# Optimization experiments

Measured on AMD Instinct MI355X. Metric: run time of the kernel, lower is better.

The kernel has to match this reference:

```python
import jax, jax.numpy as jnp
import numpy as np

B, T, D = 32, 200, 256
H, DH = 4, 32
INNER = H * DH  # 128
L, FF, NI = 8, 1024, 100000
NB = 64  # gap/recency buckets


def _ln(x, g, b, eps=1e-5):
    m = x.mean(-1, keepdims=True)
    v = jnp.mean((x - m) ** 2, -1, keepdims=True)
    return (x - m) / jnp.sqrt(v + eps) * g + b


def _gelu(x):
    return jax.nn.gelu(x, approximate=False)


def _dwconv_causal(x, w, b):
    # x: [B,T,C], w: [C,k] depthwise kernel, causal left-pad (k-1)
    k = w.shape[1]
    xp = jnp.pad(x, ((0, 0), (k - 1, 0), (0, 0))).transpose(0, 2, 1)  # [B,C,T+k-1]
    out = jax.lax.conv_general_dilated(
        xp, w[:, None, :], (1,), 'VALID',
        dimension_numbers=('NCH', 'OIH', 'NCH'), feature_group_count=w.shape[0])
    return out.transpose(0, 2, 1) + b


def _causal_linear_attention(q, k, v, m4):
    q = (jax.nn.elu(q) + 1.0) * m4
    k = (jax.nn.elu(k) + 1.0) * m4
    v = v * m4
    kv = jnp.einsum('bthd,bthe->bthde', k, v)          # [B,T,H,DH,DH]
    kv_prefix = jnp.cumsum(kv, axis=1)
    k_prefix = jnp.cumsum(k, axis=1)
    num = jnp.einsum('bthd,bthde->bthe', q, kv_prefix)
    den = jnp.sum(q * k_prefix, -1, keepdims=True)
    return num / (den + 1e-6) * m4


def _forward(item_emb, pos_emb, gap_emb, rec_emb, tf_w1, tf_b1, tf_w2, tf_b2,
             in_g, in_b, l_ln1g, l_ln1b, l_win, l_bin, l_wc, l_bc, l_tw, l_tb,
             l_pw, l_pb, l_wmix, l_bmix, l_ln2g, l_ln2b, l_wf1, l_bf1, l_wf2, l_bf2,
             fn_g, fn_b, pg_w, pg_b, uh_w1, uh_b1, uh_lng, uh_lnb, uh_w2, uh_b2,
             item_bias, ids, ts, lens):
    Bb, Tt = ids.shape
    pos = jnp.arange(Tt)
    mask = pos[None, :] >= (Tt - lens)[:, None]  # right-aligned valid mask [B,T]
    prev_ts = jnp.roll(ts, 1, axis=1)
    prev_mask = jnp.roll(mask, 1, axis=1).at[:, 0].set(False)
    zero = jnp.zeros_like(ts)
    gap_vals = jnp.where(mask & prev_mask, jnp.maximum(ts - prev_ts, 0), zero)
    latest = ts[:, -1:]
    rec_vals = jnp.where(mask, jnp.maximum(latest - ts, 0), zero)

    def buck(v, n):
        vf = jnp.maximum(v.astype(jnp.float32), 0.0)
        return jnp.clip(jnp.floor(jnp.log2(vf + 1.0)), 0, n - 1).astype(jnp.int32)

    gb = buck(gap_vals, NB)
    rb = buck(rec_vals, NB)
    rec_raw = jnp.maximum(latest - ts, 0).astype(jnp.float32)
    tf = jnp.stack([jnp.log1p(gb.astype(jnp.float32)), jnp.log1p(rec_raw)], -1)  # [B,T,2]
    dense_time = _gelu(tf @ tf_w1 + tf_b1) @ tf_w2 + tf_b2

    x = item_emb[ids] + pos_emb[None] + gap_emb[gb] + rec_emb[rb] + dense_time
    mf = mask[..., None].astype(x.dtype)
    m4 = mask[..., None, None].astype(x.dtype)
    x = _ln(x, in_g, in_b) * mf

    for i in range(L):
        res = x
        nrm = _ln(x, l_ln1g[i], l_ln1b[i])
        proj = nrm @ l_win[i] + l_bin[i]  # [B,T,D+3*INNER]
        gate = proj[..., :D]
        q = proj[..., D:D + INNER].reshape(Bb, Tt, H, DH)
        k = proj[..., D + INNER:D + 2 * INNER].reshape(Bb, Tt, H, DH)
        v = proj[..., D + 2 * INNER:].reshape(Bb, Tt, H, DH)
        content = _causal_linear_attention(q, k, v, m4).reshape(Bb, Tt, INNER) @ l_wc[i] + l_bc[i]
        temporal = _dwconv_causal(nrm, l_tw[i], l_tb[i])
        positional = _dwconv_causal(nrm, l_pw[i], l_pb[i])
        mixed = jnp.concatenate([content, temporal, positional], -1) @ l_wmix[i] + l_bmix[i]
        x = (res + jax.nn.sigmoid(gate) * mixed) * mf
        h = _ln(x, l_ln2g[i], l_ln2b[i])
        ffn = _gelu(h @ l_wf1[i] + l_bf1[i]) @ l_wf2[i] + l_bf2[i]
        x = (x + ffn) * mf

    x = _ln(x, fn_g, fn_b) * mf
    denom = jnp.maximum(lens, 1)[:, None].astype(x.dtype)
    mean_pooled = (x * mf).sum(1) / denom
    ps = (x @ pg_w + pg_b)[..., 0]
    ps = jnp.where(mask, ps, -1e9)
    pw = jax.nn.softmax(ps, axis=1)[..., None]
    attn_pooled = (pw * x).sum(1)
    last = x[:, -1, :]
    u = jnp.concatenate([last, mean_pooled, attn_pooled], -1)
    u = _gelu(u @ uh_w1 + uh_b1)
    u = _ln(u, uh_lng, uh_lnb)
    u = u @ uh_w2 + uh_b2
    u = u / jnp.maximum(jnp.linalg.norm(u, axis=-1, keepdims=True), 1e-12)
    ie = item_emb[1:]
    ie = ie / jnp.maximum(jnp.linalg.norm(ie, axis=-1, keepdims=True), 1e-12)
    return u @ ie.T + item_bias[1:]


def setup_inputs() -> dict:
    key = jax.random.key(0)
    it = iter(jax.random.split(key, 64))
    def nk():
        return next(it)
    def w(*s):
        return jax.random.normal(nk(), s, jnp.float32) * 0.02
    inp = dict(
        history_ids=jax.random.randint(nk(), (B, T), 0, NI),
        history_timestamps=jnp.sort(jax.random.randint(nk(), (B, T), 0, 1000000), axis=1),
        history_lengths=jax.random.randint(nk(), (B,), 1, T + 1),
        item_emb=w(NI + 1, D).at[0].set(0.0),
        pos_emb=w(T, D), gap_emb=w(NB, D), rec_emb=w(NB, D),
        tf_w1=w(2, D), tf_b1=jnp.zeros((D,)), tf_w2=w(D, D), tf_b2=jnp.zeros((D,)),
        in_g=jnp.ones((D,)), in_b=jnp.zeros((D,)),
        l_ln1g=jnp.ones((L, D)), l_ln1b=jnp.zeros((L, D)),
        l_win=w(L, D, D + 3 * INNER), l_bin=jnp.zeros((L, D + 3 * INNER)),
        l_wc=w(L, INNER, D), l_bc=jnp.zeros((L, D)),
        l_tw=w(L, D, 3), l_tb=jnp.zeros((L, D)),
        l_pw=w(L, D, 5), l_pb=jnp.zeros((L, D)),
        l_wmix=w(L, 3 * D, D), l_bmix=jnp.zeros((L, D)),
        l_ln2g=jnp.ones((L, D)), l_ln2b=jnp.zeros((L, D)),
        l_wf1=w(L, D, FF), l_bf1=jnp.zeros((L, FF)),
        l_wf2=w(L, FF, D), l_bf2=jnp.zeros((L, D)),
        fn_g=jnp.ones((D,)), fn_b=jnp.zeros((D,)),
        pg_w=w(D, 1), pg_b=jnp.zeros((1,)),
        uh_w1=w(3 * D, 1024), uh_b1=jnp.zeros((1024,)),
        uh_lng=jnp.ones((1024,)), uh_lnb=jnp.zeros((1024,)),
        uh_w2=w(1024, D), uh_b2=jnp.zeros((D,)),
        item_bias=jnp.zeros((NI + 1,)),
    )
    return inp


def reference(history_ids, history_timestamps, history_lengths, item_emb, pos_emb,
              gap_emb, rec_emb, tf_w1, tf_b1, tf_w2, tf_b2, in_g, in_b, l_ln1g,
              l_ln1b, l_win, l_bin, l_wc, l_bc, l_tw, l_tb, l_pw, l_pb, l_wmix,
              l_bmix, l_ln2g, l_ln2b, l_wf1, l_bf1, l_wf2, l_bf2, fn_g, fn_b,
              pg_w, pg_b, uh_w1, uh_b1, uh_lng, uh_lnb, uh_w2, uh_b2, item_bias):
    return _forward(item_emb, pos_emb, gap_emb, rec_emb, tf_w1, tf_b1, tf_w2, tf_b2,
                    in_g, in_b, l_ln1g, l_ln1b, l_win, l_bin, l_wc, l_bc, l_tw, l_tb,
                    l_pw, l_pb, l_wmix, l_bmix, l_ln2g, l_ln2b, l_wf1, l_bf1, l_wf2,
                    l_bf2, fn_g, fn_b, pg_w, pg_b, uh_w1, uh_b1, uh_lng, uh_lnb,
                    uh_w2, uh_b2, item_bias, history_ids, history_timestamps,
                    history_lengths)
```

## Files before the change

kernel.cpp:

```cpp
#include <hip/hip_runtime.h>
#include <math.h>

#define B_ 32
#define T_ 200
#define D_ 256
#define H_ 4
#define DH_ 32
#define INNER_ 128
#define L_ 8
#define FF_ 1024
#define NI_ 100000
#define NB_ 64
#define CH_ 25

typedef __attribute__((ext_vector_type(8))) short short8;
typedef __attribute__((ext_vector_type(8))) unsigned short ushort8;
typedef __attribute__((ext_vector_type(4))) unsigned short ushort4v;
typedef __attribute__((ext_vector_type(4))) float floatx4;

__device__ __forceinline__ float gelu_f(float x){
  return 0.5f*x*(1.0f+erff(x*0.70710678118654752f));
}
__device__ __forceinline__ float wsum(float v){
  #pragma unroll
  for (int o=32;o>0;o>>=1) v += __shfl_xor(v,o,64);
  return v;
}
__device__ __forceinline__ unsigned short f2bf(float x){
  unsigned int u = __float_as_uint(x);
  unsigned int r = (u + 0x7fffu + ((u>>16)&1u)) >> 16;
  return (unsigned short)r;
}
__device__ __forceinline__ float bf2f(unsigned short u){
  return __uint_as_float(((unsigned int)u)<<16);
}

__device__ __forceinline__ void cvt_tile(const float* __restrict__ src, unsigned short* __restrict__ dst,
                                         int K, int N, int tk, int tn, int tid, float (*s)[33])
{
  int tx = tid & 31, ty0 = tid >> 5;
  #pragma unroll
  for (int it=0; it<4; ++it){
    int ty = ty0 + it*8;
    s[ty][tx] = src[(size_t)(tk*32+ty)*N + tn*32+tx];
  }
  __syncthreads();
  #pragma unroll
  for (int it=0; it<4; ++it){
    int ty = ty0 + it*8;
    dst[(size_t)(tn*32+ty)*K + tk*32 + tx] = f2bf(s[tx][ty]);
  }
}

__global__ __launch_bounds__(256) void k_cvtAll(
  const float* __restrict__ win, const float* __restrict__ wmix,
  const float* __restrict__ wf1, const float* __restrict__ wf2,
  const float* __restrict__ tfw2, const float* __restrict__ uhw1, const float* __restrict__ uhw2,
  unsigned short* __restrict__ WtPerm, unsigned short* __restrict__ WtMixT,
  unsigned short* __restrict__ WtH)
{
  __shared__ float s[32][33];
  int b = blockIdx.x, tid = threadIdx.x;
  if (b < 6912){
    int l = b / 864, r = b % 864;
    if (r < 160)      cvt_tile(win + (size_t)l*163840, WtPerm + (size_t)l*688128,          256, 640,  r/20,      r%20,      tid, s);
    else if (r < 352){int t=r-160; cvt_tile(wmix + (size_t)l*196608, WtMixT + (size_t)l*196608, 768, 256, t/8, t%8, tid, s);}
    else if (r < 608){int t=r-352; cvt_tile(wf1 + (size_t)l*262144, WtPerm + (size_t)l*688128 + 163840, 256, 1024, t/32, t%32, tid, s);}
    else             {int t=r-608; cvt_tile(wf2 + (size_t)l*262144, WtPerm + (size_t)l*688128 + 425984, 1024, 256, t/8, t%8, tid, s);}
  } else {
    int r = b - 6912;
    if (r < 64)       cvt_tile(tfw2, WtH,        256, 256,  r/8,  r%8,  tid, s);
    else if (r < 832){int t=r-64;  cvt_tile(uhw1, WtH+65536,  768, 1024, t/32, t%32, tid, s);}
    else             {int t=r-832; cvt_tile(uhw2, WtH+851968, 1024, 256, t/8,  t%8,  tid, s);}
  }
}

__global__ __launch_bounds__(256) void k_asm(
  const float* __restrict__ WcombF, const unsigned short* __restrict__ WtMixT,
  unsigned short* __restrict__ WtBig)
{
  int l = blockIdx.x >> 3, g = blockIdx.x & 7;
  int tid = threadIdx.x;
  int n = g*32 + (tid >> 3);
  int k0 = (tid & 7) * 80;
  const float* wc = WcombF + (size_t)l*32768;
  const unsigned short* wm = WtMixT + (size_t)l*196608 + (size_t)n*768;
  unsigned short* dst = WtBig + (size_t)l*163840 + (size_t)n*640;
  for (int kk=0; kk<80; kk++){
    int k = k0 + kk;
    dst[k] = (k < 128) ? f2bf(wc[(size_t)k*256 + n]) : wm[k+128];
  }
}

__global__ __launch_bounds__(256) void k_bfold(
  const float* __restrict__ bc, const float* __restrict__ bmix,
  const float* __restrict__ wmix, float* __restrict__ bmixP)
{
  int l = blockIdx.x; int n = threadIdx.x;
  const float* w = wmix + (size_t)l*196608;
  const float* c = bc + l*256;
  float s = bmix[l*256 + n];
  for (int d=0; d<256; d++) s += c[d]*w[(size_t)d*256 + n];
  bmixP[l*256+n] = s;
}

template<int TN>
__global__ __launch_bounds__(256) void k_gemm_bf(
    const float* __restrict__ A, const unsigned short* __restrict__ Wt,
    const float* __restrict__ bias, float* __restrict__ C,
    int M, int N, int K, int ldA, int ldW, int ldC, int mode,
    size_t sA, size_t sW, size_t sC, size_t sB)
{
  constexpr int NJ = TN/32;
  __shared__ unsigned short Als[128][40];
  __shared__ unsigned short Bls[TN][40];
  int z = blockIdx.z;
  A += (size_t)z*sA; Wt += (size_t)z*sW; C += (size_t)z*sC;
  const float* bz = bias ? bias + (size_t)z*sB : nullptr;
  int tid = threadIdx.x;
  int wave = tid >> 6, lane = tid & 63;
  int wm = (wave >> 1) * 64, wn = (wave & 1) * (TN/2);
  int frow = lane & 15, kg = lane >> 4;
  int bm = blockIdx.y * 128, bn = blockIdx.x * TN;
  int sm = tid >> 1, skh = (tid & 1) * 16;

  floatx4 acc[4][NJ];
  #pragma unroll
  for (int i=0;i<4;i++)
    #pragma unroll
    for (int j=0;j<NJ;j++) acc[i][j] = (floatx4){0.f,0.f,0.f,0.f};

  for (int k0=0; k0<K; k0+=32){
    {
      int gm = bm + sm;
      float f[16];
      if (gm < M){
        const float4* ap = (const float4*)(A + (size_t)gm*ldA + k0 + skh);
        #pragma unroll
        for (int c=0;c<4;c++){ float4 v = ap[c]; f[c*4]=v.x; f[c*4+1]=v.y; f[c*4+2]=v.z; f[c*4+3]=v.w; }
      } else {
        #pragma unroll
        for (int c=0;c<16;c++) f[c]=0.f;
      }
      ushort8 pa, pb;
      #pragma unroll
      for (int c=0;c<8;c++){ pa[c]=f2bf(f[c]); pb[c]=f2bf(f[8+c]); }
      *(ushort8*)&Als[sm][skh]   = pa;
      *(ushort8*)&Als[sm][skh+8] = pb;
    }
    #pragma unroll
    for (int u=0; u<TN/64; u++){
      int li = tid + u*256;
      int row = li >> 2, koff = (li & 3) * 8;
      int gn = bn + row;
      ushort8 wv;
      if (gn < N){
        wv = *(const ushort8*)&Wt[(size_t)gn*ldW + k0 + koff];
      } else {
        for (int c=0;c<8;c++) wv[c]=0;
      }
      *(ushort8*)&Bls[row][koff] = wv;
    }
    __syncthreads();
    short8 af[4], bf[NJ];
    #pragma unroll
    for (int i=0;i<4;i++) af[i] = *(const short8*)&Als[wm + 16*i + frow][kg*8];
    #pragma unroll
    for (int j=0;j<NJ;j++) bf[j] = *(const short8*)&Bls[wn + 16*j + frow][kg*8];
    #pragma unroll
    for (int i=0;i<4;i++)
      #pragma unroll
      for (int j=0;j<NJ;j++)
        acc[i][j] = __builtin_amdgcn_mfma_f32_16x16x32_bf16(af[i], bf[j], acc[i][j], 0, 0, 0);
    __syncthreads();
  }

  #pragma unroll
  for (int j=0;j<NJ;j++){
    int n = bn + wn + 16*j + frow;
    float bv = bz ? bz[n] : 0.f;
    #pragma unroll
    for (int i=0;i<4;i++){
      int m0 = bm + wm + 16*i + kg*4;
      #pragma unroll
      for (int r=0;r<4;r++){
        int m = m0 + r;
        if (m < M){
          float v = acc[i][j][r] + bv;
          if (mode == 1) v = gelu_f(v);
          float* cp = &C[(size_t)m*ldC + n];
          if (mode == 2) v += *cp;
          *cp = v;
        }
      }
    }
  }
}

template<int K>
__global__ __launch_bounds__(256) void k_gemm16(
    const unsigned short* __restrict__ A, const unsigned short* __restrict__ Wt,
    const float* __restrict__ bias, void* __restrict__ Cv,
    int ldA, int ldW, int ldC, int mode)
{
  int tid = threadIdx.x;
  int wave = tid >> 6, lane = tid & 63;
  int frow = lane & 15, kg = lane >> 4;
  int bm = blockIdx.y * 32;
  int bn = blockIdx.x * 128 + wave * 32;

  const unsigned short* a0 = A + (size_t)(bm + frow)*ldA + kg*8;
  const unsigned short* a1 = a0 + (size_t)16*ldA;
  const unsigned short* b0 = Wt + (size_t)(bn + frow)*ldW + kg*8;
  const unsigned short* b1 = b0 + (size_t)16*ldW;

  floatx4 acc[2][2];
  #pragma unroll
  for (int i=0;i<2;i++)
    #pragma unroll
    for (int j=0;j<2;j++) acc[i][j] = (floatx4){0.f,0.f,0.f,0.f};

  #pragma unroll
  for (int k0=0; k0<K; k0+=32){
    short8 af0 = *(const short8*)(a0 + k0);
    short8 af1 = *(const short8*)(a1 + k0);
    short8 bf0 = *(const short8*)(b0 + k0);
    short8 bf1 = *(const short8*)(b1 + k0);
    acc[0][0] = __builtin_amdgcn_mfma_f32_16x16x32_bf16(af0, bf0, acc[0][0], 0, 0, 0);
    acc[0][1] = __builtin_amdgcn_mfma_f32_16x16x32_bf16(af0, bf1, acc[0][1], 0, 0, 0);
    acc[1][0] = __builtin_amdgcn_mfma_f32_16x16x32_bf16(af1, bf0, acc[1][0], 0, 0, 0);
    acc[1][1] = __builtin_amdgcn_mfma_f32_16x16x32_bf16(af1, bf1, acc[1][1], 0, 0, 0);
  }

  float* Cf = (float*)Cv;
  unsigned short* Ch = (unsigned short*)Cv;
  #pragma unroll
  for (int j=0;j<2;j++){
    int n = bn + 16*j + frow;
    float bv = bias[n];
    #pragma unroll
    for (int i=0;i<2;i++){
      int m0 = bm + 16*i + kg*4;
      #pragma unroll
      for (int r=0;r<4;r++){
        float v = acc[i][j][r] + bv;
        size_t off = (size_t)(m0+r)*ldC + n;
        if (mode == 1)      Cf[off] = gelu_f(v);
        else if (mode == 2) Cf[off] += v;
        else if (mode == 4) Ch[off] = f2bf(gelu_f(v));
        else                Cf[off] = v;
      }
    }
  }
}

template<int K, int MODE>
__global__ __launch_bounds__(256) void k_gemmln(
    const unsigned short* __restrict__ A, const unsigned short* __restrict__ Wt,
    const float* __restrict__ bias, float* __restrict__ xbuf,
    const float* __restrict__ gate, const int* __restrict__ lens,
    const float* __restrict__ g, const float* __restrict__ bb,
    unsigned short* __restrict__ nrm, int maskLN)
{
  __shared__ float rs[32][4];
  __shared__ float rq[32][4];
  int tid = threadIdx.x;
  int wave = tid >> 6, lane = tid & 63;
  int frow = lane & 15, kg = lane >> 4;
  int bm = blockIdx.x * 32;
  int wn = wave * 64;

  const unsigned short* a0 = A + (size_t)(bm + frow)*K + kg*8;
  const unsigned short* a1 = a0 + (size_t)16*K;
  const unsigned short* b0 = Wt + (size_t)(wn + frow)*K + kg*8;

  floatx4 acc[2][4];
  #pragma unroll
  for (int i=0;i<2;i++)
    #pragma unroll
    for (int j=0;j<4;j++) acc[i][j] = (floatx4){0.f,0.f,0.f,0.f};

  #pragma unroll
  for (int k0=0; k0<K; k0+=32){
    short8 af0 = *(const short8*)(a0 + k0);
    short8 af1 = *(const short8*)(a1 + k0);
    #pragma unroll
    for (int j=0;j<4;j++){
      short8 bf = *(const short8*)(b0 + (size_t)16*j*K + k0);
      acc[0][j] = __builtin_amdgcn_mfma_f32_16x16x32_bf16(af0, bf, acc[0][j], 0, 0, 0);
      acc[1][j] = __builtin_amdgcn_mfma_f32_16x16x32_bf16(af1, bf, acc[1][j], 0, 0, 0);
    }
  }

  float xn[2][4][4];
  float rowm[2][4];
  #pragma unroll
  for (int i=0;i<2;i++){
    #pragma unroll
    for (int r=0;r<4;r++){
      int row = bm + 16*i + kg*4 + r;
      int t = row % T_, b = row / T_;
      float m = (t >= T_ - lens[b]) ? 1.f : 0.f;
      rowm[i][r] = m;
      #pragma unroll
      for (int j=0;j<4;j++){
        int n = wn + 16*j + frow;
        float v = acc[i][j][r] + bias[n];
        float xv = xbuf[(size_t)row*256 + n];
        float xnv;
        if (MODE == 0){
          float gv = gate[(size_t)row*640 + n];
          xnv = (xv + v/(1.f+__expf(-gv)))*m;
        } else {
          xnv = (xv + v)*m;
        }
        xn[i][j][r] = xnv;
        xbuf[(size_t)row*256 + n] = xnv;
      }
    }
  }
  float mu[2][4];
  #pragma unroll
  for (int i=0;i<2;i++)
    #pragma unroll
    for (int r=0;r<4;r++){
      float s = xn[i][0][r]+xn[i][1][r]+xn[i][2][r]+xn[i][3][r];
      s += __shfl_xor(s,1,64); s += __shfl_xor(s,2,64);
      s += __shfl_xor(s,4,64); s += __shfl_xor(s,8,64);
      if (frow == 0) rs[16*i + kg*4 + r][wave] = s;
    }
  __syncthreads();
  #pragma unroll
  for (int i=0;i<2;i++)
    #pragma unroll
    for (int r=0;r<4;r++){
      int rl = 16*i + kg*4 + r;
      mu[i][r] = (rs[rl][0]+rs[rl][1]+rs[rl][2]+rs[rl][3]) * (1.f/256.f);
    }
  float rstd[2][4];
  #pragma unroll
  for (int i=0;i<2;i++)
    #pragma unroll
    for (int r=0;r<4;r++){
      float m0 = mu[i][r];
      float s = 0.f;
      #pragma unroll
      for (int j=0;j<4;j++){ float d = xn[i][j][r]-m0; s += d*d; }
      s += __shfl_xor(s,1,64); s += __shfl_xor(s,2,64);
      s += __shfl_xor(s,4,64); s += __shfl_xor(s,8,64);
      if (frow == 0) rq[16*i + kg*4 + r][wave] = s;
    }
  __syncthreads();
  #pragma unroll
  for (int i=0;i<2;i++)
    #pragma unroll
    for (int r=0;r<4;r++){
      int rl = 16*i + kg*4 + r;
      float q = rq[rl][0]+rq[rl][1]+rq[rl][2]+rq[rl][3];
      rstd[i][r] = rsqrtf(q*(1.f/256.f) + 1e-5f);
    }
  #pragma unroll
  for (int i=0;i<2;i++)
    #pragma unroll
    for (int r=0;r<4;r++){
      int row = bm + 16*i + kg*4 + r;
      float ml = maskLN ? rowm[i][r] : 1.f;
      #pragma unroll
      for (int j=0;j<4;j++){
        int n = wn + 16*j + frow;
        float h = (xn[i][j][r]-mu[i][r])*rstd[i][r]*g[n] + bb[n];
        nrm[(size_t)row*256 + n] = f2bf(h*ml);
      }
    }
}

__global__ __launch_bounds__(256) void k_embed(
  const int* __restrict__ ids, const int* __restrict__ ts, const int* __restrict__ lens,
  const float* __restrict__ item_emb, const float* __restrict__ pos_emb,
  const float* __restrict__ gap_emb, const float* __restrict__ rec_emb,
  const float* __restrict__ tf_w1, const float* __restrict__ tf_b1,
  float* __restrict__ xbuf, unsigned short* __restrict__ tfh)
{
  int bt = blockIdx.x;
  int b = bt / T_, t = bt % T_;
  int d = threadIdx.x;
  int len = lens[b];
  int tcur = ts[b*T_+t];
  int tlast = ts[b*T_+T_-1];
  bool mask  = t >= T_ - len;
  bool pmask = (t >= 1) && ((t-1) >= T_ - len);
  int gap = 0;
  if (mask && pmask){ int pv = ts[b*T_+t-1]; gap = max(tcur - pv, 0); }
  int rec = mask ? max(tlast - tcur, 0) : 0;
  int gb = min(max((int)floorf(log2f((float)gap + 1.0f)), 0), NB_-1);
  int rb = min(max((int)floorf(log2f((float)rec + 1.0f)), 0), NB_-1);
  float rec_raw = (float)max(tlast - tcur, 0);
  float tf0 = log1pf((float)gb);
  float tf1 = log1pf(rec_raw);
  float hid = gelu_f(tf0*tf_w1[d] + tf1*tf_w1[D_+d] + tf_b1[d]);
  tfh[(size_t)bt*D_ + d] = f2bf(hid);
  int id = ids[b*T_+t];
  xbuf[(size_t)bt*D_ + d] = item_emb[(size_t)id*D_ + d] + pos_emb[t*D_ + d]
                          + gap_emb[gb*D_ + d] + rec_emb[rb*D_ + d];
}

template<int NC>
__global__ __launch_bounds__(256) void k_ln(
  const float* __restrict__ in, void* __restrict__ out,
  const float* __restrict__ g, const float* __restrict__ bb,
  int rows, const int* __restrict__ lens, int applyMask, int outBf)
{
  int wid = threadIdx.x >> 6, lane = threadIdx.x & 63;
  int r = blockIdx.x*4 + wid;
  if (r >= rows) return;
  const int D = NC*256;
  const float4* rp = (const float4*)(in + (size_t)r*D);
  float4 v[NC];
  float s = 0.f;
  #pragma unroll
  for (int c=0;c<NC;c++){ v[c] = rp[c*64 + lane]; s += v[c].x+v[c].y+v[c].z+v[c].w; }
  s = wsum(s);
  float mean = s / (float)D;
  float q = 0.f;
  #pragma unroll
  for (int c=0;c<NC;c++){
    float a=v[c].x-mean, b2=v[c].y-mean, c2=v[c].z-mean, d2=v[c].w-mean;
// ... 11 lines not shown
    o.x = ((v[c].x-mean)*rstd*gg.x + bv.x)*m;
    o.y = ((v[c].y-mean)*rstd*gg.y + bv.y)*m;
    o.z = ((v[c].z-mean)*rstd*gg.z + bv.z)*m;
    o.w = ((v[c].w-mean)*rstd*gg.w + bv.w)*m;
    if (outBf){
      ushort4v ob; ob.x=f2bf(o.x); ob.y=f2bf(o.y); ob.z=f2bf(o.z); ob.w=f2bf(o.w);
      ((ushort4v*)((unsigned short*)out + (size_t)r*D))[c*64+lane] = ob;
    } else {
      ((float4*)((float*)out + (size_t)r*D))[c*64+lane] = o;
    }
  }
}

__global__ __launch_bounds__(256) void k_lnln(
  float* __restrict__ x, const int* __restrict__ lens,
  const float* __restrict__ g1, const float* __restrict__ b1,
  const float* __restrict__ g2, const float* __restrict__ b2,
  unsigned short* __restrict__ nrm)
{
  int wid = threadIdx.x >> 6, lane = threadIdx.x & 63;
  int r = blockIdx.x*4 + wid;
  int t = r % T_, b = r / T_;
  float m = (t >= T_ - lens[b]) ? 1.f : 0.f;
  float4 v = ((const float4*)(x + (size_t)r*256))[lane];
  float s = wsum(v.x+v.y+v.z+v.w);
  float mean = s/256.f;
  float a=v.x-mean, b2v=v.y-mean, c2=v.z-mean, d2=v.w-mean;
  float q = wsum(a*a+b2v*b2v+c2*c2+d2*d2);
  float rstd = rsqrtf(q/256.f + 1e-5f);
  float4 gg = ((const float4*)g1)[lane];
  float4 bv = ((const float4*)b1)[lane];
  float4 xn;
  xn.x = (a*rstd*gg.x + bv.x)*m;
  xn.y = (b2v*rstd*gg.y + bv.y)*m;
  xn.z = (c2*rstd*gg.z + bv.z)*m;
  xn.w = (d2*rstd*gg.w + bv.w)*m;
  ((float4*)(x + (size_t)r*256))[lane] = xn;
  float s2 = wsum(xn.x+xn.y+xn.z+xn.w);
  float mean2 = s2/256.f;
  float a2=xn.x-mean2, b22=xn.y-mean2, c22=xn.z-mean2, d22=xn.w-mean2;
  float q2 = wsum(a2*a2+b22*b22+c22*c22+d22*d22);
  float rstd2 = rsqrtf(q2/256.f + 1e-5f);
  float4 gg2 = ((const float4*)g2)[lane];
  float4 bv2 = ((const float4*)b2)[lane];
  ushort4v o;
  o.x = f2bf(a2*rstd2*gg2.x + bv2.x);
  o.y = f2bf(b22*rstd2*gg2.y + bv2.y);
  o.z = f2bf(c22*rstd2*gg2.z + bv2.z);
  o.w = f2bf(d22*rstd2*gg2.w + bv2.w);
  ((ushort4v*)(nrm + (size_t)r*256))[lane] = o;
}

__global__ __launch_bounds__(128) void k_attn_sums(
  const float* __restrict__ proj, const int* __restrict__ lens, float* __restrict__ Ssum)
{
  int blk = blockIdx.x;
  int bh = blk >> 3, c = blk & 7;
  int b = bh >> 2, h = bh & 3;
  int tid = threadIdx.x; int e = tid & 31, q = tid >> 5;
  int tstart = T_ - lens[b];
  __shared__ float sk[CH_*32], sv[CH_*32];
  int t0 = c*CH_;
  for (int idx = tid; idx < CH_*32; idx += 128){
    int tl = idx >> 5, dd = idx & 31;
    int t = t0 + tl;
    float m = (t >= tstart) ? 1.f : 0.f;
    const float* pr = proj + (size_t)(b*T_+t)*640 + h*32 + dd;
    float kw = pr[384], vv = pr[512];
    sk[idx] = (kw > 0.f ? kw + 1.f : __expf(kw)) * m;
    sv[idx] = vv * m;
  }
  __syncthreads();
  float acc[8];
  #pragma unroll
  for (int j=0;j<8;j++) acc[j]=0.f;
  for (int tl=0; tl<CH_; tl++){
    const float4* k4 = (const float4*)(sk + tl*32 + q*8);
    float vf = sv[tl*32 + e];
    float4 ka = k4[0], kb = k4[1];
    acc[0]+=ka.x*vf; acc[1]+=ka.y*vf; acc[2]+=ka.z*vf; acc[3]+=ka.w*vf;
    acc[4]+=kb.x*vf; acc[5]+=kb.y*vf; acc[6]+=kb.z*vf; acc[7]+=kb.w*vf;
  }
  float* dst = Ssum + ((size_t)bh*8 + c)*1056;
  #pragma unroll
  for (int j=0;j<8;j++) dst[(q*8+j)*32 + e] = acc[j];
  if (q == 0){
    float s = 0.f;
    for (int tl=0; tl<CH_; tl++) s += sk[tl*32 + e];
    dst[1024 + e] = s;
  }
}

__global__ __launch_bounds__(256) void k_dwpfx(
  const unsigned short* __restrict__ nrm, const float* __restrict__ tw, const float* __restrict__ tb,
  const float* __restrict__ pw, const float* __restrict__ pb, unsigned short* __restrict__ cat,
  float* __restrict__ Ssum)
{
  int bid = blockIdx.x;
  if (bid < 6400){
    int idx = bid*256 + threadIdx.x;
    int d = idx & 255; int bt = idx >> 8; int t = bt % T_;
    float xs[5];
    #pragma unroll
    for (int j=0;j<5;j++){
      int tt = t - 4 + j;
      xs[j] = (tt >= 0) ? bf2f(nrm[(size_t)(bt - 4 + j)*D_ + d]) : 0.f;
    }
    float tmp = tw[d*3+0]*xs[2] + tw[d*3+1]*xs[3] + tw[d*3+2]*xs[4] + tb[d];
    float pos = pb[d];
    #pragma unroll
    for (int j=0;j<5;j++) pos += pw[d*5+j]*xs[j];
    cat[(size_t)bt*640 + 128 + d] = f2bf(tmp);
    cat[(size_t)bt*640 + 384 + d] = f2bf(pos);
  } else {
    int idx = (bid - 6400)*256 + threadIdx.x;
    int bh = idx / 1056, r = idx - bh*1056;
    float* p = Ssum + (size_t)bh*8*1056 + r;
    float s = p[0];
    #pragma unroll
    for (int c=1;c<8;c++){ s += p[(size_t)c*1056]; p[(size_t)c*1056] = s; }
  }
}

__global__ __launch_bounds__(256) void k_attn_out(
  const float* __restrict__ proj, const int* __restrict__ lens,
  const float* __restrict__ Ssum, unsigned short* __restrict__ cat)
{
  int blk = blockIdx.x;
  int bh = blk >> 3, c = blk & 7;
  int b = bh >> 2, h = bh & 3;
  int tid = threadIdx.x; int e = tid & 31, qg = tid >> 5;
  int tstart = T_ - lens[b];
  __shared__ float sq[CH_*32], sk[CH_*32], sv[CH_*32];
  __shared__ float P[1056];
  __shared__ float A[CH_][CH_+1];
  __shared__ float sden[CH_];
  int t0 = c*CH_;
  if (c > 0){
    const float* Pp = Ssum + ((size_t)bh*8 + (c-1))*1056;
    for (int idx = tid; idx < 1056; idx += 256) P[idx] = Pp[idx];
  } else {
    for (int idx = tid; idx < 1056; idx += 256) P[idx] = 0.f;
  }
  for (int idx = tid; idx < CH_*32; idx += 256){
    int tl = idx >> 5, dd = idx & 31;
    int t = t0 + tl;
    float m = (t >= tstart) ? 1.f : 0.f;
    const float* pr = proj + (size_t)(b*T_+t)*640 + h*32 + dd;
    float qv = pr[256], kw = pr[384], vv = pr[512];
    sq[idx] = (qv > 0.f ? qv + 1.f : __expf(qv)) * m;
    sk[idx] = (kw > 0.f ? kw + 1.f : __expf(kw)) * m;
    sv[idx] = vv * m;
  }
  __syncthreads();
  for (int idx = tid; idx < CH_*CH_; idx += 256){
    int t = idx / CH_, tp = idx - t*CH_;
    float s = 0.f;
    if (tp <= t){
      const float4* q4 = (const float4*)(sq + t*32);
      const float4* k4 = (const float4*)(sk + tp*32);
      #pragma unroll
      for (int jj=0;jj<8;jj++){
        float4 qq = q4[jj], kk = k4[jj];
        s += qq.x*kk.x + qq.y*kk.y + qq.z*kk.z + qq.w*kk.w;
      }
    }
    A[t][tp] = s;
  }
  __syncthreads();
  if (tid < CH_){
    int t = tid;
    float s = 0.f;
    for (int tp=0; tp<=t; tp++) s += A[t][tp];
    const float* qf = sq + t*32;
    #pragma unroll
    for (int d=0; d<32; d++) s += qf[d]*P[1024+d];
    sden[t] = s;
  }
  __syncthreads();
  int tlo = (qg*CH_) >> 3, thi = ((qg+1)*CH_) >> 3;
  for (int t = tlo; t < thi; t++){
    float num = 0.f;
    for (int tp=0; tp<=t; tp++) num += A[t][tp]*sv[tp*32+e];
    const float* qf = sq + t*32;
    #pragma unroll
    for (int d=0; d<32; d++) num += qf[d]*P[d*32+e];
    int tg = t0 + t;
    float m = (tg >= tstart) ? 1.f : 0.f;
    cat[(size_t)(b*T_+tg)*640 + h*32 + e] = f2bf(num/(sden[t]+1e-6f)*m);
  }
}

__global__ __launch_bounds__(256) void k_pool(
  const unsigned short* __restrict__ x, const int* __restrict__ lens,
  const float* __restrict__ pg_w, const float* __restrict__ pg_b,
  float* __restrict__ u0)
{
  int b = blockIdx.x;
  int tid = threadIdx.x, wid = tid>>6, lane = tid&63;
  __shared__ float sps[T_];
  __shared__ float spw[T_];
  int len = lens[b]; int tstart = T_ - len;
  const float4* pw4 = (const float4*)pg_w;
  float4 wv = pw4[lane];
  for (int t = wid; t < T_; t += 4){
// ... 133 lines not shown
  const float* l_ln1g = (const float*)d_in[13];
  const float* l_ln1b = (const float*)d_in[14];
  const float* l_win  = (const float*)d_in[15];
  const float* l_bin  = (const float*)d_in[16];
  const float* l_wc   = (const float*)d_in[17];
  const float* l_bc   = (const float*)d_in[18];
  const float* l_tw   = (const float*)d_in[19];
  const float* l_tb   = (const float*)d_in[20];
  const float* l_pw   = (const float*)d_in[21];
  const float* l_pb   = (const float*)d_in[22];
  const float* l_wmix = (const float*)d_in[23];
  const float* l_bmix = (const float*)d_in[24];
  const float* l_ln2g = (const float*)d_in[25];
  const float* l_ln2b = (const float*)d_in[26];
  const float* l_wf1  = (const float*)d_in[27];
  const float* l_bf1  = (const float*)d_in[28];
  const float* l_wf2  = (const float*)d_in[29];
  const float* l_bf2  = (const float*)d_in[30];
  const float* fn_g = (const float*)d_in[31];
  const float* fn_b = (const float*)d_in[32];
  const float* pg_w = (const float*)d_in[33];
  const float* pg_b = (const float*)d_in[34];
  const float* uh_w1 = (const float*)d_in[35];
  const float* uh_b1 = (const float*)d_in[36];
  const float* uh_lng = (const float*)d_in[37];
  const float* uh_lnb = (const float*)d_in[38];
  const float* uh_w2 = (const float*)d_in[39];
  const float* uh_b2 = (const float*)d_in[40];
  const float* item_bias = (const float*)d_in[41];
  float* out = (float*)d_out;

  const int MT = B_*T_;
  float* ws   = (float*)d_ws;
  float* xbuf = ws;
  float* tmp  = xbuf + (size_t)MT*D_;
  float* proj = tmp  + (size_t)MT*D_;
  float* cat  = proj + (size_t)MT*640;
  float* mid  = cat  + (size_t)MT*640;
  float* u0   = mid  + (size_t)MT*FF_;
  float* u1   = u0 + 32*768;
  float* u2   = u1 + 32*1024;
  float* WcombF = u2 + 32*256;
  float* bmixP  = WcombF + 262144;
  float* Ssum   = bmixP + 2048;
  unsigned short* WtPerm = (unsigned short*)(Ssum + 1081344);
  unsigned short* WtMixT = WtPerm + 5505024;
  unsigned short* WtBig  = WtMixT + 1572864;
  unsigned short* WtH    = WtBig  + 1310720;
  unsigned short* u2b    = WtH    + 1114112;

  unsigned short* tmpb = (unsigned short*)tmp;
  unsigned short* catb = (unsigned short*)cat;
  unsigned short* midb = (unsigned short*)(mid + (size_t)MT*D_);

  k_cvtAll<<<8000, 256, 0, stream>>>(l_win, l_wmix, l_wf1, l_wf2, tf_w2, uh_w1, uh_w2,
                                     WtPerm, WtMixT, WtH);
  k_gemm_bf<64><<<dim3(4,1,8), 256, 0, stream>>>(l_wc, WtMixT, nullptr, WcombF,
                                                 128, 256, 256, 256, 768, 256, 0,
                                                 (size_t)128*256, (size_t)196608, (size_t)32768, 0);
  k_asm<<<64, 256, 0, stream>>>(WcombF, WtMixT, WtBig);
  k_bfold<<<8, 256, 0, stream>>>(l_bc, l_bmix, l_wmix, bmixP);

  k_embed<<<MT, 256, 0, stream>>>(ids, ts, lens, item_emb, pos_emb, gap_emb, rec_emb,
                                  tf_w1, tf_b1, xbuf, tmpb);
  k_gemm16<256><<<dim3(2,200), 256, 0, stream>>>(tmpb, WtH, tf_b2, xbuf, 256, 256, 256, 2);
  k_lnln<<<MT/4, 256, 0, stream>>>(xbuf, lens, in_g, in_b, l_ln1g, l_ln1b, tmpb);

  for (int i=0;i<L_;i++){
    const unsigned short* WL = WtPerm + (size_t)i*688128;
    k_gemm16<256><<<dim3(5,200), 256, 0, stream>>>(tmpb, WL, l_bin+i*640, proj, 256, 256, 640, 0);
    k_attn_sums<<<B_*H_*8, 128, 0, stream>>>(proj, lens, Ssum);
    k_dwpfx<<<6928, 256, 0, stream>>>(tmpb, l_tw+i*768, l_tb+i*256, l_pw+i*1280, l_pb+i*256,
                                      catb, Ssum);
    k_attn_out<<<B_*H_*8, 256, 0, stream>>>(proj, lens, Ssum, catb);
    k_gemmln<640,0><<<200, 256, 0, stream>>>(catb, WtBig+(size_t)i*163840, bmixP+i*256,
                                             xbuf, proj, lens,
                                             l_ln2g+i*256, l_ln2b+i*256, tmpb, 0);
    k_gemm16<256><<<dim3(8,200), 256, 0, stream>>>(tmpb, WL+163840, l_bf1+i*FF_, midb,
                                                   256, 256, FF_, 4);
    bool last = (i == L_-1);
    k_gemmln<1024,1><<<200, 256, 0, stream>>>(midb, WL+425984, l_bf2+i*256,
                                              xbuf, nullptr, lens,
                                              last ? fn_g : l_ln1g+(i+1)*256,
                                              last ? fn_b : l_ln1b+(i+1)*256,
                                              tmpb, last ? 1 : 0);
  }

  k_pool<<<B_, 256, 0, stream>>>(tmpb, lens, pg_w, pg_b, u0);
  k_gemm_bf<128><<<dim3(8,1), 256, 0, stream>>>(u0, WtH+65536, uh_b1, u1,
                                                32, 1024, 768, 768, 768, 1024, 1, 0,0,0,0);
  k_ln<4><<<8, 256, 0, stream>>>(u1, u1, uh_lng, uh_lnb, 32, lens, 0, 0);
  k_gemm_bf<64><<<dim3(4,1), 256, 0, stream>>>(u1, WtH+851968, uh_b2, u2,
                                               32, 256, 1024, 1024, 1024, 256, 0, 0,0,0,0);
  k_norm<<<B_, 64, 0, stream>>>(u2, u2b);

  k_score2<<<(NI_+127)/128, 256, 0, stream>>>(item_emb, u2b, item_bias, out);
}
```

Measured before the change: 1.665 ms.

## Fuse projection with feature maps and dwconv, retile GEMMs, fold bias kernel

The input projection GEMM now applies the elu+1 feature maps and masking in its epilogue. It writes gate, phiQ, phiK and V as bf16 in per-head contiguous layouts, and the same launch also computes the depthwise convolutions. The separate prefix-sum pass is dropped, and attention_out now sums the chunk states itself, which adds redundant reads for later chunks. The LN-fused GEMMs use 16-row tiles to double the block count, the FF1 GEMM gets wider N tiles per wave, and the bias-fold kernel is merged into the weight-conversion launch. Storing intermediates in bf16 cuts memory traffic but lowers precision.

```diff
diff --git a/kernel.cpp b/kernel.cpp
--- a/kernel.cpp
+++ b/kernel.cpp
@@ -57,7 +57,8 @@
   const float* __restrict__ wf1, const float* __restrict__ wf2,
   const float* __restrict__ tfw2, const float* __restrict__ uhw1, const float* __restrict__ uhw2,
   unsigned short* __restrict__ WtPerm, unsigned short* __restrict__ WtMixT,
-  unsigned short* __restrict__ WtH)
+  unsigned short* __restrict__ WtH,
+  const float* __restrict__ bc, const float* __restrict__ bmix, float* __restrict__ bmixP)
 {
   __shared__ float s[32][33];
   int b = blockIdx.x, tid = threadIdx.x;
@@ -67,11 +68,19 @@
     else if (r < 352){int t=r-160; cvt_tile(wmix + (size_t)l*196608, WtMixT + (size_t)l*196608, 768, 256, t/8, t%8, tid, s);}
     else if (r < 608){int t=r-352; cvt_tile(wf1 + (size_t)l*262144, WtPerm + (size_t)l*688128 + 163840, 256, 1024, t/32, t%32, tid, s);}
     else             {int t=r-608; cvt_tile(wf2 + (size_t)l*262144, WtPerm + (size_t)l*688128 + 425984, 1024, 256, t/8, t%8, tid, s);}
-  } else {
+  } else if (b < 8000){
     int r = b - 6912;
     if (r < 64)       cvt_tile(tfw2, WtH,        256, 256,  r/8,  r%8,  tid, s);
     else if (r < 832){int t=r-64;  cvt_tile(uhw1, WtH+65536,  768, 1024, t/32, t%32, tid, s);}
     else             {int t=r-832; cvt_tile(uhw2, WtH+851968, 1024, 256, t/8,  t%8,  tid, s);}
+  } else {
+    int l = b - 8000; int n = tid;
+    const float* w = wmix + (size_t)l*196608;
+    const float* c = bc + l*256;
+    float sum = bmix[l*256 + n];
+    #pragma unroll 8
+    for (int d=0; d<256; d++) sum += c[d]*w[(size_t)d*256 + n];
+    bmixP[l*256+n] = sum;
   }
 }
 
@@ -90,18 +99,6 @@
     int k = k0 + kk;
     dst[k] = (k < 128) ? f2bf(wc[(size_t)k*256 + n]) : wm[k+128];
   }
-}
-
-__global__ __launch_bounds__(256) void k_bfold(
-  const float* __restrict__ bc, const float* __restrict__ bmix,
-  const float* __restrict__ wmix, float* __restrict__ bmixP)
-{
-  int l = blockIdx.x; int n = threadIdx.x;
-  const float* w = wmix + (size_t)l*196608;
-  const float* c = bc + l*256;
-  float s = bmix[l*256 + n];
-  for (int d=0; d<256; d++) s += c[d]*w[(size_t)d*256 + n];
-  bmixP[l*256+n] = s;
 }
 
 template<int TN>
@@ -197,7 +194,7 @@
   }
 }
 
-template<int K>
+template<int K, int NJ>
 __global__ __launch_bounds__(256) void k_gemm16(
     const unsigned short* __restrict__ A, const unsigned short* __restrict__ Wt,
     const float* __restrict__ bias, void* __restrict__ Cv,
@@ -207,35 +204,34 @@
   int wave = tid >> 6, lane = tid & 63;
   int frow = lane & 15, kg = lane >> 4;
   int bm = blockIdx.y * 32;
-  int bn = blockIdx.x * 128 + wave * 32;
+  int bn = blockIdx.x * (64*NJ) + wave * (16*NJ);
 
   const unsigned short* a0 = A + (size_t)(bm + frow)*ldA + kg*8;
   const unsigned short* a1 = a0 + (size_t)16*ldA;
   const unsigned short* b0 = Wt + (size_t)(bn + frow)*ldW + kg*8;
-  const unsigned short* b1 = b0 + (size_t)16*ldW;
-
-  floatx4 acc[2][2];
+
+  floatx4 acc[2][NJ];
   #pragma unroll
   for (int i=0;i<2;i++)
     #pragma unroll
-    for (int j=0;j<2;j++) acc[i][j] = (floatx4){0.f,0.f,0.f,0.f};
+    for (int j=0;j<NJ;j++) acc[i][j] = (floatx4){0.f,0.f,0.f,0.f};
 
   #pragma unroll
   for (int k0=0; k0<K; k0+=32){
     short8 af0 = *(const short8*)(a0 + k0);
     short8 af1 = *(const short8*)(a1 + k0);
-    short8 bf0 = *(const short8*)(b0 + k0);
-    short8 bf1 = *(const short8*)(b1 + k0);
-    acc[0][0] = __builtin_amdgcn_mfma_f32_16x16x32_bf16(af0, bf0, acc[0][0], 0, 0, 0);
-    acc[0][1] = __builtin_amdgcn_mfma_f32_16x16x32_bf16(af0, bf1, acc[0][1], 0, 0, 0);
-    acc[1][0] = __builtin_amdgcn_mfma_f32_16x16x32_bf16(af1, bf0, acc[1][0], 0, 0, 0);
-    acc[1][1] = __builtin_amdgcn_mfma_f32_16x16x32_bf16(af1, bf1, acc[1][1], 0, 0, 0);
+    #pragma unroll
+    for (int j=0;j<NJ;j++){
+      short8 bf = *(const short8*)(b0 + (size_t)j*16*ldW + k0);
+      acc[0][j] = __builtin_amdgcn_mfma_f32_16x16x32_bf16(af0, bf, acc[0][j], 0, 0, 0);
+      acc[1][j] = __builtin_amdgcn_mfma_f32_16x16x32_bf16(af1, bf, acc[1][j], 0, 0, 0);
+    }
   }
 
   float* Cf = (float*)Cv;
   unsigned short* Ch = (unsigned short*)Cv;
   #pragma unroll
-  for (int j=0;j<2;j++){
+  for (int j=0;j<NJ;j++){
     int n = bn + 16*j + frow;
     float bv = bias[n];
     #pragma unroll
@@ -254,124 +250,195 @@
   }
 }
 
+__global__ __launch_bounds__(256) void k_proj(
+  const unsigned short* __restrict__ A, const unsigned short* __restrict__ Wt,
+  const float* __restrict__ bias, const int* __restrict__ lens,
+  unsigned short* __restrict__ gateb, unsigned short* __restrict__ phiQ,
+  unsigned short* __restrict__ phiK, unsigned short* __restrict__ vB,
+  const float* __restrict__ tw, const float* __restrict__ tb,
+  const float* __restrict__ pw, const float* __restrict__ pb,
+  unsigned short* __restrict__ cat)
+{
+  int bid = blockIdx.x;
+  int tid = threadIdx.x;
+  if (bid < 400){
+    int wave = tid >> 6, lane = tid & 63;
+    int frow = lane & 15, kg = lane >> 4;
+    int bx = bid & 1, by = bid >> 1;
+    int bm = by * 32;
+    int wn = bx*320 + wave*80;
+    const unsigned short* a0 = A + (size_t)(bm + frow)*256 + kg*8;
+    const unsigned short* a1 = a0 + (size_t)16*256;
+    const unsigned short* b0 = Wt + (size_t)(wn + frow)*256 + kg*8;
+    floatx4 acc[2][5];
+    #pragma unroll
+    for (int i=0;i<2;i++)
+      #pragma unroll
+      for (int j=0;j<5;j++) acc[i][j] = (floatx4){0.f,0.f,0.f,0.f};
+    #pragma unroll
+    for (int k0=0; k0<256; k0+=32){
+      short8 af0 = *(const short8*)(a0 + k0);
+      short8 af1 = *(const short8*)(a1 + k0);
+      #pragma unroll
+      for (int j=0;j<5;j++){
+        short8 bf = *(const short8*)(b0 + (size_t)j*16*256 + k0);
+        acc[0][j] = __builtin_amdgcn_mfma_f32_16x16x32_bf16(af0, bf, acc[0][j], 0, 0, 0);
+        acc[1][j] = __builtin_amdgcn_mfma_f32_16x16x32_bf16(af1, bf, acc[1][j], 0, 0, 0);
+      }
+    }
+    #pragma unroll
+    for (int i=0;i<2;i++){
+      #pragma unroll
+      for (int r=0;r<4;r++){
+        int row = bm + 16*i + kg*4 + r;
+        int t = row % T_, b = row / T_;
+        float m = (t >= T_ - lens[b]) ? 1.f : 0.f;
+        #pragma unroll
+        for (int j=0;j<5;j++){
+          int n = wn + 16*j + frow;
+          float v = acc[i][j][r] + bias[n];
+          if (n < 256){
+            gateb[(size_t)row*256 + n] = f2bf(v);
+          } else if (n < 384){
+            int bh = b*4 + ((n-256)>>5), dd = n & 31;
+            phiQ[(size_t)bh*6400 + t*32 + dd] = f2bf((v > 0.f ? v + 1.f : __expf(v))*m);
+          } else if (n < 512){
+            int bh = b*4 + ((n-384)>>5), dd = n & 31;
+            phiK[(size_t)bh*6400 + t*32 + dd] = f2bf((v > 0.f ? v + 1.f : __expf(v))*m);
+          } else {
+            int bh = b*4 + ((n-512)>>5), dd = n & 31;
+            vB[(size_t)bh*6400 + t*32 + dd] = f2bf(v*m);
+          }
+        }
+      }
+    }
+  } else {
+    int bid2 = bid - 400;
+    int d = tid;
+    int bt0 = bid2*4;
+    float xs8[8];
+    #pragma unroll
+    for (int w=0;w<8;w++){
+      int wr = bt0 - 4 + w;
+      xs8[w] = (wr >= 0) ? bf2f(A[(size_t)wr*256 + d]) : 0.f;
+    }
+    #pragma unroll
+    for (int rr=0;rr<4;rr++){
+      int bt = bt0 + rr, t = bt % T_;
+      float ot = tb[d], op = pb[d];
+      #pragma unroll
+      for (int j=0;j<5;j++){
+        int tt = t - 4 + j;
+        float xv = (tt >= 0) ? xs8[rr+j] : 0.f;
+        op += pw[d*5+j]*xv;
+        if (j >= 2) ot += tw[d*3 + (j-2)]*xv;
+      }
+      cat[(size_t)bt*640 + 128 + d] = f2bf(ot);
+      cat[(size_t)bt*640 + 384 + d] = f2bf(op);
+    }
+  }
+}
+
 template<int K, int MODE>
 __global__ __launch_bounds__(256) void k_gemmln(
     const unsigned short* __restrict__ A, const unsigned short* __restrict__ Wt,
     const float* __restrict__ bias, float* __restrict__ xbuf,
-    const float* __restrict__ gate, const int* __restrict__ lens,
+    const unsigned short* __restrict__ gateb, const int* __restrict__ lens,
     const float* __restrict__ g, const float* __restrict__ bb,
     unsigned short* __restrict__ nrm, int maskLN)
 {
-  __shared__ float rs[32][4];
-  __shared__ float rq[32][4];
+  __shared__ float rs[16][4];
+  __shared__ float rq[16][4];
   int tid = threadIdx.x;
   int wave = tid >> 6, lane = tid & 63;
   int frow = lane & 15, kg = lane >> 4;
-  int bm = blockIdx.x * 32;
+  int bm = blockIdx.x * 16;
   int wn = wave * 64;
 
   const unsigned short* a0 = A + (size_t)(bm + frow)*K + kg*8;
-  const unsigned short* a1 = a0 + (size_t)16*K;
   const unsigned short* b0 = Wt + (size_t)(wn + frow)*K + kg*8;
 
-  floatx4 acc[2][4];
-  #pragma unroll
-  for (int i=0;i<2;i++)
-    #pragma unroll
-    for (int j=0;j<4;j++) acc[i][j] = (floatx4){0.f,0.f,0.f,0.f};
+  floatx4 acc[4];
+  #pragma unroll
+  for (int j=0;j<4;j++) acc[j] = (floatx4){0.f,0.f,0.f,0.f};
 
   #pragma unroll
   for (int k0=0; k0<K; k0+=32){
     short8 af0 = *(const short8*)(a0 + k0);
-    short8 af1 = *(const short8*)(a1 + k0);
     #pragma unroll
     for (int j=0;j<4;j++){
       short8 bf = *(const short8*)(b0 + (size_t)16*j*K + k0);
-      acc[0][j] = __builtin_amdgcn_mfma_f32_16x16x32_bf16(af0, bf, acc[0][j], 0, 0, 0);
-      acc[1][j] = __builtin_amdgcn_mfma_f32_16x16x32_bf16(af1, bf, acc[1][j], 0, 0, 0);
-    }
-  }
-
-  float xn[2][4][4];
-  float rowm[2][4];
-  #pragma unroll
-  for (int i=0;i<2;i++){
-    #pragma unroll
-    for (int r=0;r<4;r++){
-      int row = bm + 16*i + kg*4 + r;
-      int t = row % T_, b = row / T_;
-      float m = (t >= T_ - lens[b]) ? 1.f : 0.f;
-      rowm[i][r] = m;
-      #pragma unroll
-      for (int j=0;j<4;j++){
-        int n = wn + 16*j + frow;
-        float v = acc[i][j][r] + bias[n];
-        float xv = xbuf[(size_t)row*256 + n];
-        float xnv;
-        if (MODE == 0){
-          float gv = gate[(size_t)row*640 + n];
-          xnv = (xv + v/(1.f+__expf(-gv)))*m;
-        } else {
-          xnv = (xv + v)*m;
-        }
-        xn[i][j][r] = xnv;
-        xbuf[(size_t)row*256 + n] = xnv;
+      acc[j] = __builtin_amdgcn_mfma_f32_16x16x32_bf16(af0, bf, acc[j], 0, 0, 0);
+    }
+  }
+
+  float xn[4][4];
+  float rowm[4];
+  #pragma unroll
+  for (int r=0;r<4;r++){
+    int row = bm + kg*4 + r;
+    int t = row % T_, b = row / T_;
+    float m = (t >= T_ - lens[b]) ? 1.f : 0.f;
+    rowm[r] = m;
+    #pragma unroll
+    for (int j=0;j<4;j++){
+      int n = wn + 16*j + frow;
+      float v = acc[j][r] + bias[n];
+      float xv = xbuf[(size_t)row*256 + n];
+      float xnv;
+      if (MODE == 0){
+        float gv = bf2f(gateb[(size_t)row*256 + n]);
+        xnv = (xv + v/(1.f+__expf(-gv)))*m;
+      } else {
+        xnv = (xv + v)*m;
       }
-    }
-  }
-  float mu[2][4];
-  #pragma unroll
-  for (int i=0;i<2;i++)
-    #pragma unroll
-    for (int r=0;r<4;r++){
-      float s = xn[i][0][r]+xn[i][1][r]+xn[i][2][r]+xn[i][3][r];
-      s += __shfl_xor(s,1,64); s += __shfl_xor(s,2,64);
-      s += __shfl_xor(s,4,64); s += __shfl_xor(s,8,64);
-      if (frow == 0) rs[16*i + kg*4 + r][wave] = s;
-    }
+      xn[j][r] = xnv;
+      xbuf[(size_t)row*256 + n] = xnv;
+    }
+  }
+  float mu[4];
+  #pragma unroll
+  for (int r=0;r<4;r++){
+    float s = xn[0][r]+xn[1][r]+xn[2][r]+xn[3][r];
+    s += __shfl_xor(s,1,64); s += __shfl_xor(s,2,64);
+    s += __shfl_xor(s,4,64); s += __shfl_xor(s,8,64);
+    if (frow == 0) rs[kg*4 + r][wave] = s;
+  }
   __syncthreads();
   #pragma unroll
-  for (int i=0;i<2;i++)
-    #pragma unroll
-    for (int r=0;r<4;r++){
-      int rl = 16*i + kg*4 + r;
-      mu[i][r] = (rs[rl][0]+rs[rl][1]+rs[rl][2]+rs[rl][3]) * (1.f/256.f);
-    }
-  float rstd[2][4];
-  #pragma unroll
-  for (int i=0;i<2;i++)
-    #pragma unroll
-    for (int r=0;r<4;r++){
-      float m0 = mu[i][r];
-      float s = 0.f;
-      #pragma unroll
-      for (int j=0;j<4;j++){ float d = xn[i][j][r]-m0; s += d*d; }
-      s += __shfl_xor(s,1,64); s += __shfl_xor(s,2,64);
-      s += __shfl_xor(s,4,64); s += __shfl_xor(s,8,64);
-      if (frow == 0) rq[16*i + kg*4 + r][wave] = s;
-    }
+  for (int r=0;r<4;r++){
+    int rl = kg*4 + r;
+    mu[r] = (rs[rl][0]+rs[rl][1]+rs[rl][2]+rs[rl][3]) * (1.f/256.f);
+  }
+  float rstd[4];
+  #pragma unroll
+  for (int r=0;r<4;r++){
+    float m0 = mu[r];
+    float s = 0.f;
+    #pragma unroll
+    for (int j=0;j<4;j++){ float d = xn[j][r]-m0; s += d*d; }
+    s += __shfl_xor(s,1,64); s += __shfl_xor(s,2,64);
+    s += __shfl_xor(s,4,64); s += __shfl_xor(s,8,64);
+    if (frow == 0) rq[kg*4 + r][wave] = s;
+  }
   __syncthreads();
   #pragma unroll
-  for (int i=0;i<2;i++)
-    #pragma unroll
-    for (int r=0;r<4;r++){
-      int rl = 16*i + kg*4 + r;
-      float q = rq[rl][0]+rq[rl][1]+rq[rl][2]+rq[rl][3];
-      rstd[i][r] = rsqrtf(q*(1.f/256.f) + 1e-5f);
-    }
-  #pragma unroll
-  for (int i=0;i<2;i++)
-    #pragma unroll
-    for (int r=0;r<4;r++){
-      int row = bm + 16*i + kg*4 + r;
-      float ml = maskLN ? rowm[i][r] : 1.f;
-      #pragma unroll
-      for (int j=0;j<4;j++){
-        int n = wn + 16*j + frow;
-        float h = (xn[i][j][r]-mu[i][r])*rstd[i][r]*g[n] + bb[n];
-        nrm[(size_t)row*256 + n] = f2bf(h*ml);
-      }
-    }
+  for (int r=0;r<4;r++){
+    int rl = kg*4 + r;
+    float q = rq[rl][0]+rq[rl][1]+rq[rl][2]+rq[rl][3];
+    rstd[r] = rsqrtf(q*(1.f/256.f) + 1e-5f);
+  }
+  #pragma unroll
+  for (int r=0;r<4;r++){
+    int row = bm + kg*4 + r;
+    float ml = maskLN ? rowm[r] : 1.f;
+    #pragma unroll
+    for (int j=0;j<4;j++){
+      int n = wn + 16*j + frow;
+      float h = (xn[j][r]-mu[r])*rstd[r]*g[n] + bb[n];
+      nrm[(size_t)row*256 + n] = f2bf(h*ml);
+    }
+  }
 }
 
 __global__ __launch_bounds__(256) void k_embed(
@@ -489,23 +556,17 @@
 }
 
 __global__ __launch_bounds__(128) void k_attn_sums(
-  const float* __restrict__ proj, const int* __restrict__ lens, float* __restrict__ Ssum)
+  const unsigned short* __restrict__ phiK, const unsigned short* __restrict__ vB,
+  float* __restrict__ Ssum)
 {
   int blk = blockIdx.x;
   int bh = blk >> 3, c = blk & 7;
-  int b = bh >> 2, h = bh & 3;
   int tid = threadIdx.x; int e = tid & 31, q = tid >> 5;
-  int tstart = T_ - lens[b];
   __shared__ float sk[CH_*32], sv[CH_*32];
-  int t0 = c*CH_;
+  size_t base = (size_t)bh*6400 + (size_t)c*CH_*32;
   for (int idx = tid; idx < CH_*32; idx += 128){
-    int tl = idx >> 5, dd = idx & 31;
-    int t = t0 + tl;
-    float m = (t >= tstart) ? 1.f : 0.f;
-    const float* pr = proj + (size_t)(b*T_+t)*640 + h*32 + dd;
-    float kw = pr[384], vv = pr[512];
-    sk[idx] = (kw > 0.f ? kw + 1.f : __expf(kw)) * m;
-    sv[idx] = vv * m;
+    sk[idx] = bf2f(phiK[base + idx]);
+    sv[idx] = bf2f(vB[base + idx]);
   }
   __syncthreads();
   float acc[8];
@@ -528,39 +589,9 @@
   }
 }
 
-__global__ __launch_bounds__(256) void k_dwpfx(
-  const unsigned short* __restrict__ nrm, const float* __restrict__ tw, const float* __restrict__ tb,
-  const float* __restrict__ pw, const float* __restrict__ pb, unsigned short* __restrict__ cat,
-  float* __restrict__ Ssum)
-{
-  int bid = blockIdx.x;
-  if (bid < 6400){
-    int idx = bid*256 + threadIdx.x;
-    int d = idx & 255; int bt = idx >> 8; int t = bt % T_;
-    float xs[5];
-    #pragma unroll
-    for (int j=0;j<5;j++){
-      int tt = t - 4 + j;
-      xs[j] = (tt >= 0) ? bf2f(nrm[(size_t)(bt - 4 + j)*D_ + d]) : 0.f;
-    }
-    float tmp = tw[d*3+0]*xs[2] + tw[d*3+1]*xs[3] + tw[d*3+2]*xs[4] + tb[d];
-    float pos = pb[d];
-    #pragma unroll
-    for (int j=0;j<5;j++) pos += pw[d*5+j]*xs[j];
-    cat[(size_t)bt*640 + 128 + d] = f2bf(tmp);
-    cat[(size_t)bt*640 + 384 + d] = f2bf(pos);
-  } else {
-    int idx = (bid - 6400)*256 + threadIdx.x;
-    int bh = idx / 1056, r = idx - bh*1056;
-    float* p = Ssum + (size_t)bh*8*1056 + r;
-    float s = p[0];
-    #pragma unroll
-    for (int c=1;c<8;c++){ s += p[(size_t)c*1056]; p[(size_t)c*1056] = s; }
-  }
-}
-
 __global__ __launch_bounds__(256) void k_attn_out(
-  const float* __restrict__ proj, const int* __restrict__ lens,
+  const unsigned short* __restrict__ phiQ, const unsigned short* __restrict__ phiK,
+  const unsigned short* __restrict__ vB, const int* __restrict__ lens,
   const float* __restrict__ Ssum, unsigned short* __restrict__ cat)
 {
   int blk = blockIdx.x;
@@ -573,21 +604,17 @@
   __shared__ float A[CH_][CH_+1];
   __shared__ float sden[CH_];
   int t0 = c*CH_;
-  if (c > 0){
-    const float* Pp = Ssum + ((size_t)bh*8 + (c-1))*1056;
-    for (int idx = tid; idx < 1056; idx += 256) P[idx] = Pp[idx];
-  } else {
-    for (int idx = tid; idx < 1056; idx += 256) P[idx] = 0.f;
-  }
+  const float* basep = Ssum + (size_t)bh*8*1056;
+  for (int idx = tid; idx < 1056; idx += 256){
+    float s = 0.f;
+    for (int cp=0; cp<c; cp++) s += basep[(size_t)cp*1056 + idx];
+    P[idx] = s;
+  }
+  size_t base = (size_t)bh*6400 + (size_t)c*CH_*32;
   for (int idx = tid; idx < CH_*32; idx += 256){
-    int tl = idx >> 5, dd = idx & 31;
-    int t = t0 + tl;
-    float m = (t >= tstart) ? 1.f : 0.f;
-    const float* pr = proj + (size_t)(b*T_+t)*640 + h*32 + dd;
-    float qv = pr[256], kw = pr[384], vv = pr[512];
-    sq[idx] = (qv > 0.f ? qv + 1.f : __expf(qv)) * m;
-    sk[idx] = (kw > 0.f ? kw + 1.f : __expf(kw)) * m;
-    sv[idx] = vv * m;
+    sq[idx] = bf2f(phiQ[base + idx]);
+    sk[idx] = bf2f(phiK[base + idx]);
+    sv[idx] = bf2f(vB[base + idx]);
   }
   __syncthreads();
   for (int idx = tid; idx < CH_*CH_; idx += 256){
@@ -827,34 +854,37 @@
   unsigned short* tmpb = (unsigned short*)tmp;
   unsigned short* catb = (unsigned short*)cat;
   unsigned short* midb = (unsigned short*)(mid + (size_t)MT*D_);
-
-  k_cvtAll<<<8000, 256, 0, stream>>>(l_win, l_wmix, l_wf1, l_wf2, tf_w2, uh_w1, uh_w2,
-                                     WtPerm, WtMixT, WtH);
+  unsigned short* gateb = (unsigned short*)proj;
+  unsigned short* phiQ  = gateb + 1638400;
+  unsigned short* phiK  = phiQ + 819200;
+  unsigned short* vBuf  = phiK + 819200;
+
+  k_cvtAll<<<8008, 256, 0, stream>>>(l_win, l_wmix, l_wf1, l_wf2, tf_w2, uh_w1, uh_w2,
+                                     WtPerm, WtMixT, WtH, l_bc, l_bmix, bmixP);
   k_gemm_bf<64><<<dim3(4,1,8), 256, 0, stream>>>(l_wc, WtMixT, nullptr, WcombF,
                                                  128, 256, 256, 256, 768, 256, 0,
                                                  (size_t)128*256, (size_t)196608, (size_t)32768, 0);
   k_asm<<<64, 256, 0, stream>>>(WcombF, WtMixT, WtBig);
-  k_bfold<<<8, 256, 0, stream>>>(l_bc, l_bmix, l_wmix, bmixP);
 
   k_embed<<<MT, 256, 0, stream>>>(ids, ts, lens, item_emb, pos_emb, gap_emb, rec_emb,
                                   tf_w1, tf_b1, xbuf, tmpb);
-  k_gemm16<256><<<dim3(2,200), 256, 0, stream>>>(tmpb, WtH, tf_b2, xbuf, 256, 256, 256, 2);
+  k_gemm16<256,2><<<dim3(2,200), 256, 0, stream>>>(tmpb, WtH, tf_b2, xbuf, 256, 256, 256, 2);
   k_lnln<<<MT/4, 256, 0, stream>>>(xbuf, lens, in_g, in_b, l_ln1g, l_ln1b, tmpb);
 
   for (int i=0;i<L_;i++){
     const unsigned short* WL = WtPerm + (size_t)i*688128;
-    k_gemm16<256><<<dim3(5,200), 256, 0, stream>>>(tmpb, WL, l_bin+i*640, proj, 256, 256, 640, 0);
-    k_attn_sums<<<B_*H_*8, 128, 0, stream>>>(proj, lens, Ssum);
-    k_dwpfx<<<6928, 256, 0, stream>>>(tmpb, l_tw+i*768, l_tb+i*256, l_pw+i*1280, l_pb+i*256,
-                                      catb, Ssum);
-    k_attn_out<<<B_*H_*8, 256, 0, stream>>>(proj, lens, Ssum, catb);
-    k_gemmln<640,0><<<200, 256, 0, stream>>>(catb, WtBig+(size_t)i*163840, bmixP+i*256,
-                                             xbuf, proj, lens,
+    k_proj<<<2000, 256, 0, stream>>>(tmpb, WL, l_bin+i*640, lens,
+                                     gateb, phiQ, phiK, vBuf,
+                                     l_tw+i*768, l_tb+i*256, l_pw+i*1280, l_pb+i*256, catb);
+    k_attn_sums<<<B_*H_*8, 128, 0, stream>>>(phiK, vBuf, Ssum);
+    k_attn_out<<<B_*H_*8, 256, 0, stream>>>(phiQ, phiK, vBuf, lens, Ssum, catb);
+    k_gemmln<640,0><<<400, 256, 0, stream>>>(catb, WtBig+(size_t)i*163840, bmixP+i*256,
+                                             xbuf, gateb, lens,
                                              l_ln2g+i*256, l_ln2b+i*256, tmpb, 0);
-    k_gemm16<256><<<dim3(8,200), 256, 0, stream>>>(tmpb, WL+163840, l_bf1+i*FF_, midb,
-                                                   256, 256, FF_, 4);
+    k_gemm16<256,4><<<dim3(4,200), 256, 0, stream>>>(tmpb, WL+163840, l_bf1+i*FF_, midb,
+                                                     256, 256, FF_, 4);
     bool last = (i == L_-1);
-    k_gemmln<1024,1><<<200, 256, 0, stream>>>(midb, WL+425984, l_bf2+i*256,
+    k_gemmln<1024,1><<<400, 256, 0, stream>>>(midb, WL+425984, l_bf2+i*256,
                                               xbuf, nullptr, lens,
                                               last ? fn_g : l_ln1g+(i+1)*256,
                                               last ? fn_b : l_ln1b+(i+1)*256,
```

Result: no change. 1.687 ms (+1.3%).
